# Optimization experiments

Measured on AMD Instinct MI355X. Metric: run time of the kernel, lower is better.

Reference implementation:

```python
import jax, jax.numpy as jnp
import numpy as np

N, E, D, H = 10000, 160000, 128, 4  # nodes, edges, node/edge dim, heads
HC = H * D  # 512, concat output dim of TransformerConv
LN_EPS = 1e-5


def setup_inputs() -> dict:
    key = jax.random.key(0)
    ks = jax.random.split(key, 16)
    s = 1.0 / np.sqrt(D)
    s2 = 1.0 / np.sqrt(HC)
    return {
        "x": jax.random.normal(ks[0], (N, D), jnp.float32),
        "edge_index": jax.random.randint(ks[1], (2, E), 0, N, jnp.int64),
        "edge_attr": jax.random.normal(ks[2], (E, D), jnp.float32),
        "Wq": jax.random.normal(ks[3], (D, HC), jnp.float32) * s,
        "bq": jnp.zeros((HC,), jnp.float32),
        "Wk": jax.random.normal(ks[4], (D, HC), jnp.float32) * s,
        "bk": jnp.zeros((HC,), jnp.float32),
        "Wv": jax.random.normal(ks[5], (D, HC), jnp.float32) * s,
        "bv": jnp.zeros((HC,), jnp.float32),
        "We": jax.random.normal(ks[6], (D, HC), jnp.float32) * s,
        "be": jnp.zeros((HC,), jnp.float32),
        "Wskip": jax.random.normal(ks[7], (D, HC), jnp.float32) * s,
        "bskip": jnp.zeros((HC,), jnp.float32),
        "ln_g": jnp.ones((HC,), jnp.float32),
        "ln_b": jnp.zeros((HC,), jnp.float32),
        "Wlin": jax.random.normal(ks[8], (HC, D), jnp.float32) * s2,
        "blin": jnp.zeros((D,), jnp.float32),
    }


def reference(x, edge_index, edge_attr, Wq, bq, Wk, bk, Wv, bv, We, be,
              Wskip, bskip, ln_g, ln_b, Wlin, blin):
    n = x.shape[0]
    src, dst = edge_index[0], edge_index[1]  # message flows src -> dst
    q = (x @ Wq + bq).reshape(n, H, D)
    k = (x @ Wk + bk).reshape(n, H, D)
    v = (x @ Wv + bv).reshape(n, H, D)
    e = (edge_attr @ We + be).reshape(-1, H, D)  # [E,H,D]

    kj = k[src] + e                                   # [E,H,D]
    alpha = jnp.einsum('ehd,ehd->eh', q[dst], kj) / np.sqrt(D)  # [E,H]
    # per-destination-node, per-head softmax over incoming edges
    amax = jax.ops.segment_max(alpha, dst, num_segments=n)      # [N,H]
    ex = jnp.exp(alpha - amax[dst])
    denom = jax.ops.segment_sum(ex, dst, num_segments=n)        # [N,H]
    attn = ex / denom[dst]                                      # [E,H]

    msg = (v[src] + e) * attn[:, :, None]                       # [E,H,D]
    agg = jax.ops.segment_sum(msg, dst, num_segments=n).reshape(n, HC)
    out = agg + (x @ Wskip + bskip)  # root/skip connection (concat heads)

    # LayerNorm over H*D
    mu = out.mean(-1, keepdims=True)
    var = ((out - mu) ** 2).mean(-1, keepdims=True)
    normed = (out - mu) * jax.lax.rsqrt(var + LN_EPS) * ln_g + ln_b

    lin = normed @ Wlin + blin
    return jax.nn.elu(lin + x)
```

## Files before the change

kernel.cpp:

```cpp
#include <hip/hip_runtime.h>
#include <math.h>


typedef short bf16x8 __attribute__((ext_vector_type(8)));
typedef unsigned short u16x8 __attribute__((ext_vector_type(8)));
typedef float f32x4 __attribute__((ext_vector_type(4)));

#define SCALE 0.08838834764831845f

__device__ inline unsigned short f2bf(float f) {
    union { float f; unsigned u; } v; v.f = f;
    unsigned r = (v.u + 0x7FFFu + ((v.u >> 16) & 1u)) >> 16;
    return (unsigned short)r;
}
__device__ inline float bf2f(unsigned short u) {
    union { unsigned u; float f; } v; v.u = ((unsigned)u) << 16; return v.f;
}

__global__ __launch_bounds__(256) void wqe_k(
    const float* __restrict__ Wq, const float* __restrict__ bq,
    const float* __restrict__ We,
    float* __restrict__ WqeT, float* __restrict__ bqe)
{
    const int b = blockIdx.x;
    if (b < 256) {
        const int gid = b * 256 + threadIdx.x;
        const int m = gid >> 9, hc = gid & 511;
        const int h = hc >> 7, c = hc & 127;
        const float* wq = &Wq[(size_t)m * 512 + h * 128];
        const float* we = &We[(size_t)c * 512 + h * 128];
        float s0 = 0.f, s1 = 0.f;
        #pragma unroll 8
        for (int d = 0; d < 128; d += 2) { s0 += wq[d] * we[d]; s1 += wq[d + 1] * we[d + 1]; }
        WqeT[(size_t)m * 512 + hc] = (s0 + s1) * SCALE;
    } else {
        const int hc = (b - 256) * 256 + threadIdx.x;
        const int h = hc >> 7, c = hc & 127;
        const float* we = &We[(size_t)c * 512 + h * 128];
        const float* bb = &bq[h * 128];
        float s = 0.f;
        #pragma unroll 8
        for (int d = 0; d < 128; ++d) s += bb[d] * we[d];
        bqe[hc] = s * SCALE;
    }
}

__global__ __launch_bounds__(256) void prep_k(
    const float* __restrict__ x,
    const float* __restrict__ Wq, const float* __restrict__ bq,
    const float* __restrict__ Wk, const float* __restrict__ bk,
    const float* __restrict__ Wv, const float* __restrict__ bv,
    const float* __restrict__ Ws, const float* __restrict__ bs,
    const float* __restrict__ WqeT, const float* __restrict__ bqe,
    const float* __restrict__ We, const float* __restrict__ Wlin,
    unsigned short* __restrict__ x_bf, unsigned short* __restrict__ Wfrag,
    unsigned short* __restrict__ Wefrag, unsigned short* __restrict__ Wlfrag,
    float* __restrict__ bcat, int n, int nb1)
{
    const int b = blockIdx.x, t = threadIdx.x;
    if (b < nb1) {
        int i = (b * 256 + t) * 4;
        if (i < n * 128) {
            float4 v = *(const float4*)&x[i];
            unsigned short o[4] = { f2bf(v.x), f2bf(v.y), f2bf(v.z), f2bf(v.w) };
            *(uint2*)&x_bf[i] = *(uint2*)o;
        }
    } else if (b < nb1 + 160) {
        int g = (b - nb1) * 256 + t;
        int lane = g & 63, kt = (g >> 6) & 3, nt = g >> 8;
        int ncol = nt * 16 + (lane & 15);
        int k0 = kt * 32 + ((lane >> 4) << 3);
        const float* W; int c; float sc = 1.f;
        if      (ncol < 512)  { W = Wq;   c = ncol; sc = SCALE; }
        else if (ncol < 1024) { W = Wk;   c = ncol - 512; }
        else if (ncol < 1536) { W = Wv;   c = ncol - 1024; }
        else if (ncol < 2048) { W = Ws;   c = ncol - 1536; }
        else                  { W = WqeT; c = ncol - 2048; }
        unsigned short o[8];
        #pragma unroll
        for (int j = 0; j < 8; ++j) o[j] = f2bf(W[(size_t)(k0 + j) * 512 + c] * sc);
        *(uint4*)&Wfrag[(size_t)g * 8] = *(uint4*)o;
    } else if (b < nb1 + 192) {
        int g = (b - nb1 - 160) * 256 + t;
        int lane = g & 63, kt = (g >> 6) & 3, nt = g >> 8;
        int ncol = nt * 16 + (lane & 15);
        int k0 = kt * 32 + ((lane >> 4) << 3);
        unsigned short o[8];
        #pragma unroll
        for (int j = 0; j < 8; ++j) o[j] = f2bf(We[(size_t)(k0 + j) * 512 + ncol]);
        *(uint4*)&Wefrag[(size_t)g * 8] = *(uint4*)o;
    } else if (b < nb1 + 224) {
        int g = (b - nb1 - 192) * 256 + t;
        int lane = g & 63, kt = (g >> 6) & 15, nt = g >> 10;
        int ncol = nt * 16 + (lane & 15);
        int k0 = kt * 32 + ((lane >> 4) << 3);
        unsigned short o[8];
        #pragma unroll
        for (int j = 0; j < 8; ++j) o[j] = f2bf(Wlin[(size_t)(k0 + j) * 128 + ncol]);
        *(uint4*)&Wlfrag[(size_t)g * 8] = *(uint4*)o;
    } else {
        int c = (b - nb1 - 224) * 256 + t;
        if (c < 2560)
            bcat[c] = (c < 512) ? bq[c] * SCALE : (c < 1024) ? bk[c - 512]
                     : (c < 1536) ? bv[c - 1024] : (c < 2048) ? bs[c - 1536] : bqe[c - 2048];
    }
}

__global__ __launch_bounds__(256) void node_gemm_mfma(
    const unsigned short* __restrict__ x_bf, const unsigned short* __restrict__ Wfrag,
    const float* __restrict__ bcat, float* __restrict__ qs,
    unsigned short* __restrict__ kvq, int n)
{
    const int t = threadIdx.x, lane = t & 63, w = t >> 6;
    const int m0 = blockIdx.x * 64 + (w >> 1) * 32;
    const int n0 = blockIdx.y * 64 + (w & 1) * 32;
    const int lr = lane & 15, lk = (lane >> 4) << 3;
    f32x4 acc[2][2] = {};
    #pragma unroll
    for (int kt = 0; kt < 4; ++kt) {
        bf16x8 a[2], bf[2];
        #pragma unroll
        for (int mi = 0; mi < 2; ++mi) {
            int row = m0 + mi * 16 + lr; row = row < n ? row : n - 1;
            a[mi] = *(const bf16x8*)&x_bf[(size_t)row * 128 + kt * 32 + lk];
        }
        #pragma unroll
        for (int ni = 0; ni < 2; ++ni) {
            int nt = (n0 + ni * 16) >> 4;
            bf[ni] = *(const bf16x8*)&Wfrag[(size_t)((nt * 4 + kt) * 64 + lane) * 8];
        }
        #pragma unroll
        for (int mi = 0; mi < 2; ++mi)
            #pragma unroll
            for (int ni = 0; ni < 2; ++ni)
                acc[mi][ni] = __builtin_amdgcn_mfma_f32_16x16x32_bf16(a[mi], bf[ni], acc[mi][ni], 0, 0, 0);
    }
    #pragma unroll
    for (int mi = 0; mi < 2; ++mi)
        #pragma unroll
        for (int j = 0; j < 4; ++j) {
            int row = m0 + mi * 16 + (lane >> 4) * 4 + j;
            if (row < n) {
                #pragma unroll
                for (int ni = 0; ni < 2; ++ni) {
                    int col = n0 + ni * 16 + lr;
                    float val = acc[mi][ni][j] + bcat[col];
                    if (col < 1536)       kvq[(size_t)row * 2048 + col] = f2bf(val);
                    else if (col < 2048)  qs[(size_t)row * 512 + col - 1536] = val;
                    else                  kvq[(size_t)row * 2048 + col - 512] = f2bf(val);
                }
            }
        }
}

__global__ void deg_count_k(const int* __restrict__ dst, int* __restrict__ deg, int E)
{
    int e = blockIdx.x * 256 + threadIdx.x;
    if (e < E) atomicAdd(&deg[dst[e]], 1);
}

__global__ __launch_bounds__(1024) void scan_k(const int* __restrict__ deg,
                                               int* __restrict__ row_start,
                                               int* __restrict__ cursor, int n)
{
    __shared__ int part[1024];
    const int t = threadIdx.x;
    const int c0 = t * 16;
    int loc[16];
    int s = 0;
    #pragma unroll
    for (int i = 0; i < 16; ++i) {
        int idx = c0 + i;
        int dv = (idx < n) ? deg[idx] : 0;
        loc[i] = s; s += dv;
    }
    part[t] = s;
    __syncthreads();
    int incl = s;
    for (int off = 1; off < 1024; off <<= 1) {
        int other = (t >= off) ? part[t - off] : 0;
        __syncthreads();
        incl += other;
        part[t] = incl;
        __syncthreads();
    }
    const int base = incl - s;
    #pragma unroll
    for (int i = 0; i < 16; ++i) {
        int idx = c0 + i;
        if (idx < n) { row_start[idx] = base + loc[i]; cursor[idx] = base + loc[i]; }
    }
    if (t == 1023) row_start[n] = incl;
}

__global__ void scatter_k(const int* __restrict__ ei, int* __restrict__ cursor,
                          int2* __restrict__ csr, int E)
{
    int e = blockIdx.x * 256 + threadIdx.x;
    if (e < E) {
        int dnode = ei[E + e];
        int p = atomicAdd(&cursor[dnode], 1);
        csr[p] = make_int2(e, ei[e]);
    }
}

__global__ __launch_bounds__(256) void edge_k(
    const unsigned short* __restrict__ kvq, const float* __restrict__ ea,
    const float* __restrict__ be,
    const int* __restrict__ row_start, const int2* __restrict__ csr,
    unsigned short* __restrict__ wsum_bf, unsigned short* __restrict__ vacc_bf, int n)
{
    const int t = threadIdx.x, lane = t & 63, w = t >> 6;
    const int slot = w >> 1, half = w & 1;
    const int node = blockIdx.x * 2 + slot;
    const bool nvalid = node < n;
    const int nodec = nvalid ? node : 0;
    const int g = lane >> 4;
    const int l15 = lane & 15;
    const int sl = l15 * 8;

    __shared__ float lds_m[2][4], lds_den[2][4];
    __shared__ float lds_va[2][4][128], lds_ws[2][4][128];

    int rs = 0, deg = 0;
    if (nvalid) { rs = row_start[node]; deg = row_start[node + 1] - rs; }
    const int dh = (deg + 1) >> 1;
    const int lo = half ? dh : 0;
    const int myc = half ? (deg - dh) : dh;

    float q8[8], qe8[8];
    {
        const u16x8 uq  = *(const u16x8*)&kvq[(size_t)nodec * 2048 + g * 128 + sl];
        const u16x8 uqe = *(const u16x8*)&kvq[(size_t)nodec * 2048 + 1536 + g * 128 + sl];
        #pragma unroll
        for (int i = 0; i < 8; ++i) { q8[i] = bf2f(uq[i]); qe8[i] = bf2f(uqe[i]); }
    }
    float qbe;
    {
        const float* bp = &be[g * 128 + sl];
        float pb = 0.f;
        #pragma unroll
        for (int i = 0; i < 8; ++i) pb += q8[i] * bp[i];
        #pragma unroll
        for (int o = 1; o <= 8; o <<= 1) pb += __shfl_xor(pb, o);
        qbe = pb;
    }

    float m = -3.0e38f, den = 0.f;
    float va[8] = {}, ws[8] = {};

    for (int j0 = 0; j0 < myc; j0 += 64) {
        const int cnt = min(64, myc - j0);
        int2 my = make_int2(0, 0);
        if (lane < cnt) my = csr[rs + lo + j0 + lane];
        for (int jj = 0; jj < cnt; jj += 2) {
            const bool two = (jj + 1 < cnt);
            const int j1 = two ? jj + 1 : jj;
            const int eid0 = __shfl(my.x, jj), src0 = __shfl(my.y, jj);
            const int eid1 = __shfl(my.x, j1), src1 = __shfl(my.y, j1);
            const float* ep0 = &ea[(size_t)eid0 * 128 + sl];
            const float* ep1 = &ea[(size_t)eid1 * 128 + sl];
            float4 eA0 = *(const float4*)ep0, eB0 = *(const float4*)(ep0 + 4);
            float4 eA1 = *(const float4*)ep1, eB1 = *(const float4*)(ep1 + 4);
            const u16x8 k0 = *(const u16x8*)&kvq[(size_t)src0 * 2048 + 512 + g * 128 + sl];
            const u16x8 v0 = *(const u16x8*)&kvq[(size_t)src0 * 2048 + 1024 + g * 128 + sl];
            const u16x8 k1 = *(const u16x8*)&kvq[(size_t)src1 * 2048 + 512 + g * 128 + sl];
            const u16x8 v1 = *(const u16x8*)&kvq[(size_t)src1 * 2048 + 1024 + g * 128 + sl];
            float ef0[8] = {eA0.x, eA0.y, eA0.z, eA0.w, eB0.x, eB0.y, eB0.z, eB0.w};
            float ef1[8] = {eA1.x, eA1.y, eA1.z, eA1.w, eB1.x, eB1.y, eB1.z, eB1.w};
            float p0 = 0.f, p1 = 0.f;
            #pragma unroll
            for (int i = 0; i < 8; ++i) {
                p0 += q8[i] * bf2f(k0[i]) + qe8[i] * ef0[i];
                p1 += q8[i] * bf2f(k1[i]) + qe8[i] * ef1[i];
            }
            #pragma unroll
            for (int o = 1; o <= 8; o <<= 1) {
                p0 += __shfl_xor(p0, o);
                p1 += __shfl_xor(p1, o);
            }
            const float a0 = p0 + qbe;
            const float a1 = two ? (p1 + qbe) : -3.0e38f;
            const float gm = fmaxf(a0, a1);
            if (gm > m + 8.f) {
                const float sc = __expf(m - gm);
                den *= sc;
                #pragma unroll
                for (int i = 0; i < 8; ++i) { va[i] *= sc; ws[i] *= sc; }
                m = gm;
            }
            const float w0 = __expf(a0 - m);
            const float w1 = __expf(a1 - m);
            den += w0 + w1;
            #pragma unroll
            for (int i = 0; i < 8; ++i) {
                va[i] += w0 * bf2f(v0[i]) + w1 * bf2f(v1[i]);
                ws[i] += w0 * ef0[i] + w1 * ef1[i];
            }
        }
    }

    if (half == 1) {
        if (l15 == 0) { lds_m[slot][g] = m; lds_den[slot][g] = den; }
        #pragma unroll
        for (int i = 0; i < 8; ++i) {
            lds_va[slot][g][sl + i] = va[i];
            lds_ws[slot][g][sl + i] = ws[i];
        }
    }
    __syncthreads();
    if (half == 0 && nvalid) {
        const float m1 = lds_m[slot][g], den1 = lds_den[slot][g];
        const float M = fmaxf(m, m1);
        const float s0 = __expf(m - M), s1 = __expf(m1 - M);
        const float dtot = den * s0 + den1 * s1;
        const float rden = (dtot > 0.f) ? 1.f / dtot : 0.f;
        unsigned short vo[8], wo[8];
        #pragma unroll
        for (int i = 0; i < 8; ++i) {
            vo[i] = f2bf((va[i] * s0 + lds_va[slot][g][sl + i] * s1) * rden);
            wo[i] = f2bf((ws[i] * s0 + lds_ws[slot][g][sl + i] * s1) * rden);
        }
        *(uint4*)&vacc_bf[(size_t)node * 512 + g * 128 + sl] = *(uint4*)vo;
        *(uint4*)&wsum_bf[(size_t)node * 512 + g * 128 + sl] = *(uint4*)wo;
    }
}

__global__ __launch_bounds__(256) void tail_k(
    const unsigned short* __restrict__ wsum_bf, const unsigned short* __restrict__ Wefrag,
    const float* __restrict__ be, const unsigned short* __restrict__ vacc_bf,
    const float* __restrict__ qs, const int* __restrict__ row_start,
    const unsigned short* __restrict__ Wlfrag, const float* __restrict__ lng,
    const float* __restrict__ lnb, const float* __restrict__ blin,
    const float* __restrict__ x, float* __restrict__ out, int n)
{
    const int t = threadIdx.x, lane = t & 63, w = t >> 6;
    const int r0 = blockIdx.x * 16;
    const int lr = lane & 15, lk = (lane >> 4) << 3;
    __shared__ unsigned short nlds[16][520];
    __shared__ float red_s[4][16], red_q[4][16], mval[16], rval[16];

    f32x4 acc[8] = {};
    #pragma unroll
    for (int kt = 0; kt < 4; ++kt) {
        int row = r0 + lr; row = row < n ? row : n - 1;
        bf16x8 a = *(const bf16x8*)&wsum_bf[(size_t)row * 512 + w * 128 + kt * 32 + lk];
        #pragma unroll
        for (int ni = 0; ni < 8; ++ni) {
            bf16x8 bfr = *(const bf16x8*)&Wefrag[(size_t)(((w * 8 + ni) * 4 + kt) * 64 + lane) * 8];
            acc[ni] = __builtin_amdgcn_mfma_f32_16x16x32_bf16(a, bfr, acc[ni], 0, 0, 0);
        }
    }
    float g8[8], b8[8];
    #pragma unroll
    for (int ni = 0; ni < 8; ++ni) { int col = w * 128 + ni * 16 + lr; g8[ni] = lng[col]; b8[ni] = lnb[col]; }
    float sum_[4], sq_[4];
    #pragma unroll
    for (int j = 0; j < 4; ++j) {
        int row = r0 + (lane >> 4) * 4 + j;
        int rowc = row < n ? row : n - 1;
        const float hb = (row_start[rowc + 1] > row_start[rowc]) ? 1.f : 0.f;
        float s = 0.f, q = 0.f;
        #pragma unroll
        for (int ni = 0; ni < 8; ++ni) {
            int col = w * 128 + ni * 16 + lr;
            float y = acc[ni][j] + bf2f(vacc_bf[(size_t)rowc * 512 + col]) + hb * be[col]
                    + qs[(size_t)rowc * 512 + col];
            acc[ni][j] = y;
            s += y; q += y * y;
        }
        sum_[j] = s; sq_[j] = q;
    }
    #pragma unroll
    for (int o = 1; o <= 8; o <<= 1) {
        #pragma unroll
        for (int j = 0; j < 4; ++j) { sum_[j] += __shfl_xor(sum_[j], o); sq_[j] += __shfl_xor(sq_[j], o); }
    }
    if (lr == 0) {
        #pragma unroll
        for (int j = 0; j < 4; ++j) {
            red_s[w][(lane >> 4) * 4 + j] = sum_[j];
            red_q[w][(lane >> 4) * 4 + j] = sq_[j];
        }
    }
    __syncthreads();
    if (t < 16) {
        float S = red_s[0][t] + red_s[1][t] + red_s[2][t] + red_s[3][t];
        float Q = red_q[0][t] + red_q[1][t] + red_q[2][t] + red_q[3][t];
        float mu = S * (1.f / 512.f);
        float var = Q * (1.f / 512.f) - mu * mu;
        mval[t] = mu;
        rval[t] = rsqrtf(fmaxf(var, 0.f) + 1e-5f);
    }
    __syncthreads();
    #pragma unroll
    for (int j = 0; j < 4; ++j) {
        int rowl = (lane >> 4) * 4 + j;
        float mu = mval[rowl], rv = rval[rowl];
        #pragma unroll
        for (int ni = 0; ni < 8; ++ni) {
            int col = w * 128 + ni * 16 + lr;
            nlds[rowl][col] = f2bf((acc[ni][j] - mu) * rv * g8[ni] + b8[ni]);
        }
    }
    __syncthreads();
    f32x4 acc2[2] = {};
    #pragma unroll
    for (int kt = 0; kt < 16; ++kt) {
        bf16x8 a2 = *(const bf16x8*)&nlds[lr][kt * 32 + lk];
        #pragma unroll
        for (int ni = 0; ni < 2; ++ni) {
            bf16x8 bfr = *(const bf16x8*)&Wlfrag[(size_t)(((w * 2 + ni) * 16 + kt) * 64 + lane) * 8];
            acc2[ni] = __builtin_amdgcn_mfma_f32_16x16x32_bf16(a2, bfr, acc2[ni], 0, 0, 0);
        }
    }
    #pragma unroll
    for (int j = 0; j < 4; ++j) {
        int row = r0 + (lane >> 4) * 4 + j;
        if (row < n) {
            #pragma unroll
            for (int ni = 0; ni < 2; ++ni) {
                int col = w * 32 + ni * 16 + lr;
                float z = acc2[ni][j] + blin[col] + x[(size_t)row * 128 + col];
                out[(size_t)row * 128 + col] = z > 0.f ? z : expm1f(z);
            }
        }
    }
}

extern "C" void kernel_launch(void* const* d_in, const int* in_sizes, int n_in,
                              void* d_out, int out_size, void* d_ws, size_t ws_size,
                              hipStream_t stream)
{
    const float* x   = (const float*)d_in[0];
    const int*   ei  = (const int*)d_in[1];
    const float* ea  = (const float*)d_in[2];
    const float* Wq  = (const float*)d_in[3];
    const float* bq  = (const float*)d_in[4];
    const float* Wk  = (const float*)d_in[5];
    const float* bk  = (const float*)d_in[6];
    const float* Wv  = (const float*)d_in[7];
    const float* bv  = (const float*)d_in[8];
    const float* We  = (const float*)d_in[9];
    const float* be  = (const float*)d_in[10];
    const float* Wsk = (const float*)d_in[11];
    const float* bsk = (const float*)d_in[12];
    const float* lng = (const float*)d_in[13];
    const float* lnb = (const float*)d_in[14];
    const float* Wl  = (const float*)d_in[15];
    const float* bl  = (const float*)d_in[16];
    float* out = (float*)d_out;

    const int n = in_sizes[0] / 128;
    const int E = in_sizes[1] / 2;

    float* qs    = (float*)d_ws;
    float* WqeT  = qs + (size_t)n * 512;
    float* bqe   = WqeT + 128 * 512;
    float* bcat  = bqe + 512;
    unsigned short* x_bf    = (unsigned short*)(bcat + 2560);
    unsigned short* wsum_bf = x_bf + (size_t)n * 128;
    unsigned short* vacc_bf = wsum_bf + (size_t)n * 512;
    unsigned short* kvq     = vacc_bf + (size_t)n * 512;
    unsigned short* Wfrag   = kvq + (size_t)n * 2048;
    unsigned short* Wefrag  = Wfrag + 128 * 2560;
    unsigned short* Wlfrag  = Wefrag + 128 * 512;
    int2* csr = (int2*)(((uintptr_t)(Wlfrag + 512 * 128) + 7) & ~(uintptr_t)7);
    int* deg       = (int*)(csr + E);
    int* row_start = deg + n;
    int* cursor    = row_start + n + 1;

    hipMemsetAsync(deg, 0, (size_t)n * sizeof(int), stream);

    wqe_k<<<258, 256, 0, stream>>>(Wq, bq, We, WqeT, bqe);
    const int nb1 = (n * 32 + 255) / 256;
    prep_k<<<nb1 + 234, 256, 0, stream>>>(x, Wq, bq, Wk, bk, Wv, bv, Wsk, bsk, WqeT, bqe,
                                          We, Wl, x_bf, Wfrag, Wefrag, Wlfrag, bcat, n, nb1);
    dim3 g1((n + 63) / 64, 40);
    node_gemm_mfma<<<g1, 256, 0, stream>>>(x_bf, Wfrag, bcat, qs, kvq, n);
    deg_count_k<<<(E + 255) / 256, 256, 0, stream>>>(ei + E, deg, E);
    scan_k<<<1, 1024, 0, stream>>>(deg, row_start, cursor, n);
    scatter_k<<<(E + 255) / 256, 256, 0, stream>>>(ei, cursor, csr, E);
    edge_k<<<(n + 1) / 2, 256, 0, stream>>>(kvq, ea, be, row_start, csr,
                                            wsum_bf, vacc_bf, n);
    tail_k<<<(n + 15) / 16, 256, 0, stream>>>(wsum_bf, Wefrag, be, vacc_bf, qs, row_start,
                                              Wlfrag, lng, lnb, bl, x, out, n);
}
```

Measured before the change: 181.2 us.

## Fold CSR build into existing kernels and unroll edge loop by four

```diff
diff --git a/kernel.cpp b/kernel.cpp
--- a/kernel.cpp
+++ b/kernel.cpp
@@ -20,7 +20,8 @@
 __global__ __launch_bounds__(256) void wqe_k(
     const float* __restrict__ Wq, const float* __restrict__ bq,
     const float* __restrict__ We,
-    float* __restrict__ WqeT, float* __restrict__ bqe)
+    float* __restrict__ WqeT, float* __restrict__ bqe,
+    int* __restrict__ deg, int n)
 {
     const int b = blockIdx.x;
     if (b < 256) {
@@ -33,7 +34,7 @@
         #pragma unroll 8
         for (int d = 0; d < 128; d += 2) { s0 += wq[d] * we[d]; s1 += wq[d + 1] * we[d + 1]; }
         WqeT[(size_t)m * 512 + hc] = (s0 + s1) * SCALE;
-    } else {
+    } else if (b < 258) {
         const int hc = (b - 256) * 256 + threadIdx.x;
         const int h = hc >> 7, c = hc & 127;
         const float* we = &We[(size_t)c * 512 + h * 128];
@@ -42,6 +43,9 @@
         #pragma unroll 8
         for (int d = 0; d < 128; ++d) s += bb[d] * we[d];
         bqe[hc] = s * SCALE;
+    } else {
+        int idx = (b - 258) * 256 + threadIdx.x;
+        if (idx < n) deg[idx] = 0;
     }
 }
 
@@ -55,7 +59,8 @@
     const float* __restrict__ We, const float* __restrict__ Wlin,
     unsigned short* __restrict__ x_bf, unsigned short* __restrict__ Wfrag,
     unsigned short* __restrict__ Wefrag, unsigned short* __restrict__ Wlfrag,
-    float* __restrict__ bcat, int n, int nb1)
+    float* __restrict__ bcat,
+    const int* __restrict__ ei, int* __restrict__ deg, int E, int n, int nb1)
 {
     const int b = blockIdx.x, t = threadIdx.x;
     if (b < nb1) {
@@ -98,19 +103,67 @@
         #pragma unroll
         for (int j = 0; j < 8; ++j) o[j] = f2bf(Wlin[(size_t)(k0 + j) * 128 + ncol]);
         *(uint4*)&Wlfrag[(size_t)g * 8] = *(uint4*)o;
-    } else {
+    } else if (b < nb1 + 234) {
         int c = (b - nb1 - 224) * 256 + t;
         if (c < 2560)
             bcat[c] = (c < 512) ? bq[c] * SCALE : (c < 1024) ? bk[c - 512]
                      : (c < 1536) ? bv[c - 1024] : (c < 2048) ? bs[c - 1536] : bqe[c - 2048];
-    }
+    } else {
+        int e = (b - nb1 - 234) * 256 + t;
+        if (e < E) atomicAdd(&deg[ei[E + e]], 1);
+    }
+}
+
+__global__ __launch_bounds__(1024) void scan_k(const int* __restrict__ deg,
+                                               int* __restrict__ row_start,
+                                               int* __restrict__ cursor, int n)
+{
+    __shared__ int part[1024];
+    const int t = threadIdx.x;
+    const int c0 = t * 16;
+    int loc[16];
+    int s = 0;
+    #pragma unroll
+    for (int i = 0; i < 16; ++i) {
+        int idx = c0 + i;
+        int dv = (idx < n) ? deg[idx] : 0;
+        loc[i] = s; s += dv;
+    }
+    part[t] = s;
+    __syncthreads();
+    int incl = s;
+    for (int off = 1; off < 1024; off <<= 1) {
+        int other = (t >= off) ? part[t - off] : 0;
+        __syncthreads();
+        incl += other;
+        part[t] = incl;
+        __syncthreads();
+    }
+    const int base = incl - s;
+    #pragma unroll
+    for (int i = 0; i < 16; ++i) {
+        int idx = c0 + i;
+        if (idx < n) { row_start[idx] = base + loc[i]; cursor[idx] = base + loc[i]; }
+    }
+    if (t == 1023) row_start[n] = incl;
 }
 
 __global__ __launch_bounds__(256) void node_gemm_mfma(
     const unsigned short* __restrict__ x_bf, const unsigned short* __restrict__ Wfrag,
     const float* __restrict__ bcat, float* __restrict__ qs,
-    unsigned short* __restrict__ kvq, int n)
-{
+    unsigned short* __restrict__ kvq,
+    const int* __restrict__ ei, int* __restrict__ cursor, int2* __restrict__ csr,
+    int E, int n)
+{
+    if (blockIdx.y == 40) {
+        const int nth = gridDim.x * 256;
+        for (int e = blockIdx.x * 256 + threadIdx.x; e < E; e += nth) {
+            int dnode = ei[E + e];
+            int p = atomicAdd(&cursor[dnode], 1);
+            csr[p] = make_int2(e, ei[e]);
+        }
+        return;
+    }
     const int t = threadIdx.x, lane = t & 63, w = t >> 6;
     const int m0 = blockIdx.x * 64 + (w >> 1) * 32;
     const int n0 = blockIdx.y * 64 + (w & 1) * 32;
@@ -153,58 +206,7 @@
         }
 }
 
-__global__ void deg_count_k(const int* __restrict__ dst, int* __restrict__ deg, int E)
-{
-    int e = blockIdx.x * 256 + threadIdx.x;
-    if (e < E) atomicAdd(&deg[dst[e]], 1);
-}
-
-__global__ __launch_bounds__(1024) void scan_k(const int* __restrict__ deg,
-                                               int* __restrict__ row_start,
-                                               int* __restrict__ cursor, int n)
-{
-    __shared__ int part[1024];
-    const int t = threadIdx.x;
-    const int c0 = t * 16;
-    int loc[16];
-    int s = 0;
-    #pragma unroll
-    for (int i = 0; i < 16; ++i) {
-        int idx = c0 + i;
-        int dv = (idx < n) ? deg[idx] : 0;
-        loc[i] = s; s += dv;
-    }
-    part[t] = s;
-    __syncthreads();
-    int incl = s;
-    for (int off = 1; off < 1024; off <<= 1) {
-        int other = (t >= off) ? part[t - off] : 0;
-        __syncthreads();
-        incl += other;
-        part[t] = incl;
-        __syncthreads();
-    }
-    const int base = incl - s;
-    #pragma unroll
-    for (int i = 0; i < 16; ++i) {
-        int idx = c0 + i;
-        if (idx < n) { row_start[idx] = base + loc[i]; cursor[idx] = base + loc[i]; }
-    }
-    if (t == 1023) row_start[n] = incl;
-}
-
-__global__ void scatter_k(const int* __restrict__ ei, int* __restrict__ cursor,
-                          int2* __restrict__ csr, int E)
-{
-    int e = blockIdx.x * 256 + threadIdx.x;
-    if (e < E) {
-        int dnode = ei[E + e];
-        int p = atomicAdd(&cursor[dnode], 1);
-        csr[p] = make_int2(e, ei[e]);
-    }
-}
-
-__global__ __launch_bounds__(256) void edge_k(
+__global__ __launch_bounds__(256, 4) void edge_k(
     const unsigned short* __restrict__ kvq, const float* __restrict__ ea,
     const float* __restrict__ be,
     const int* __restrict__ row_start, const int2* __restrict__ csr,
@@ -253,35 +255,51 @@
         const int cnt = min(64, myc - j0);
         int2 my = make_int2(0, 0);
         if (lane < cnt) my = csr[rs + lo + j0 + lane];
-        for (int jj = 0; jj < cnt; jj += 2) {
-            const bool two = (jj + 1 < cnt);
-            const int j1 = two ? jj + 1 : jj;
-            const int eid0 = __shfl(my.x, jj), src0 = __shfl(my.y, jj);
-            const int eid1 = __shfl(my.x, j1), src1 = __shfl(my.y, j1);
-            const float* ep0 = &ea[(size_t)eid0 * 128 + sl];
-            const float* ep1 = &ea[(size_t)eid1 * 128 + sl];
-            float4 eA0 = *(const float4*)ep0, eB0 = *(const float4*)(ep0 + 4);
-            float4 eA1 = *(const float4*)ep1, eB1 = *(const float4*)(ep1 + 4);
-            const u16x8 k0 = *(const u16x8*)&kvq[(size_t)src0 * 2048 + 512 + g * 128 + sl];
-            const u16x8 v0 = *(const u16x8*)&kvq[(size_t)src0 * 2048 + 1024 + g * 128 + sl];
-            const u16x8 k1 = *(const u16x8*)&kvq[(size_t)src1 * 2048 + 512 + g * 128 + sl];
-            const u16x8 v1 = *(const u16x8*)&kvq[(size_t)src1 * 2048 + 1024 + g * 128 + sl];
-            float ef0[8] = {eA0.x, eA0.y, eA0.z, eA0.w, eB0.x, eB0.y, eB0.z, eB0.w};
-            float ef1[8] = {eA1.x, eA1.y, eA1.z, eA1.w, eB1.x, eB1.y, eB1.z, eB1.w};
-            float p0 = 0.f, p1 = 0.f;
+        for (int jj = 0; jj < cnt; jj += 4) {
+            const int i1 = min(jj + 1, cnt - 1), i2 = min(jj + 2, cnt - 1), i3 = min(jj + 3, cnt - 1);
+            const bool b1 = jj + 1 < cnt, b2 = jj + 2 < cnt, b3 = jj + 3 < cnt;
+            const int e0 = __shfl(my.x, jj), s0_ = __shfl(my.y, jj);
+            const int e1 = __shfl(my.x, i1), s1_ = __shfl(my.y, i1);
+            const int e2 = __shfl(my.x, i2), s2_ = __shfl(my.y, i2);
+            const int e3 = __shfl(my.x, i3), s3_ = __shfl(my.y, i3);
+            const float* ep0 = &ea[(size_t)e0 * 128 + sl];
+            const float* ep1 = &ea[(size_t)e1 * 128 + sl];
+            const float* ep2 = &ea[(size_t)e2 * 128 + sl];
+            const float* ep3 = &ea[(size_t)e3 * 128 + sl];
+            float4 A0 = *(const float4*)ep0, B0 = *(const float4*)(ep0 + 4);
+            float4 A1 = *(const float4*)ep1, B1 = *(const float4*)(ep1 + 4);
+            float4 A2 = *(const float4*)ep2, B2 = *(const float4*)(ep2 + 4);
+            float4 A3 = *(const float4*)ep3, B3 = *(const float4*)(ep3 + 4);
+            const u16x8 K0 = *(const u16x8*)&kvq[(size_t)s0_ * 2048 + 512 + g * 128 + sl];
+            const u16x8 V0 = *(const u16x8*)&kvq[(size_t)s0_ * 2048 + 1024 + g * 128 + sl];
+            const u16x8 K1 = *(const u16x8*)&kvq[(size_t)s1_ * 2048 + 512 + g * 128 + sl];
+            const u16x8 V1 = *(const u16x8*)&kvq[(size_t)s1_ * 2048 + 1024 + g * 128 + sl];
+            const u16x8 K2 = *(const u16x8*)&kvq[(size_t)s2_ * 2048 + 512 + g * 128 + sl];
+            const u16x8 V2 = *(const u16x8*)&kvq[(size_t)s2_ * 2048 + 1024 + g * 128 + sl];
+            const u16x8 K3 = *(const u16x8*)&kvq[(size_t)s3_ * 2048 + 512 + g * 128 + sl];
+            const u16x8 V3 = *(const u16x8*)&kvq[(size_t)s3_ * 2048 + 1024 + g * 128 + sl];
+            float ef0[8] = {A0.x, A0.y, A0.z, A0.w, B0.x, B0.y, B0.z, B0.w};
+            float ef1[8] = {A1.x, A1.y, A1.z, A1.w, B1.x, B1.y, B1.z, B1.w};
+            float ef2[8] = {A2.x, A2.y, A2.z, A2.w, B2.x, B2.y, B2.z, B2.w};
+            float ef3[8] = {A3.x, A3.y, A3.z, A3.w, B3.x, B3.y, B3.z, B3.w};
+            float p0 = 0.f, p1 = 0.f, p2 = 0.f, p3 = 0.f;
             #pragma unroll
             for (int i = 0; i < 8; ++i) {
-                p0 += q8[i] * bf2f(k0[i]) + qe8[i] * ef0[i];
-                p1 += q8[i] * bf2f(k1[i]) + qe8[i] * ef1[i];
+                p0 += q8[i] * bf2f(K0[i]) + qe8[i] * ef0[i];
+                p1 += q8[i] * bf2f(K1[i]) + qe8[i] * ef1[i];
+                p2 += q8[i] * bf2f(K2[i]) + qe8[i] * ef2[i];
+                p3 += q8[i] * bf2f(K3[i]) + qe8[i] * ef3[i];
             }
             #pragma unroll
             for (int o = 1; o <= 8; o <<= 1) {
-                p0 += __shfl_xor(p0, o);
-                p1 += __shfl_xor(p1, o);
+                p0 += __shfl_xor(p0, o); p1 += __shfl_xor(p1, o);
+                p2 += __shfl_xor(p2, o); p3 += __shfl_xor(p3, o);
             }
             const float a0 = p0 + qbe;
-            const float a1 = two ? (p1 + qbe) : -3.0e38f;
-            const float gm = fmaxf(a0, a1);
+            const float a1 = b1 ? (p1 + qbe) : -3.0e38f;
+            const float a2 = b2 ? (p2 + qbe) : -3.0e38f;
+            const float a3 = b3 ? (p3 + qbe) : -3.0e38f;
+            const float gm = fmaxf(fmaxf(a0, a1), fmaxf(a2, a3));
             if (gm > m + 8.f) {
                 const float sc = __expf(m - gm);
                 den *= sc;
@@ -291,11 +309,13 @@
             }
             const float w0 = __expf(a0 - m);
             const float w1 = __expf(a1 - m);
-            den += w0 + w1;
+            const float w2 = __expf(a2 - m);
+            const float w3 = __expf(a3 - m);
+            den += (w0 + w1) + (w2 + w3);
             #pragma unroll
             for (int i = 0; i < 8; ++i) {
-                va[i] += w0 * bf2f(v0[i]) + w1 * bf2f(v1[i]);
-                ws[i] += w0 * ef0[i] + w1 * ef1[i];
+                va[i] += (w0 * bf2f(V0[i]) + w1 * bf2f(V1[i])) + (w2 * bf2f(V2[i]) + w3 * bf2f(V3[i]));
+                ws[i] += (w0 * ef0[i] + w1 * ef1[i]) + (w2 * ef2[i] + w3 * ef3[i]);
             }
         }
     }
@@ -470,17 +490,16 @@
     int* row_start = deg + n;
     int* cursor    = row_start + n + 1;
 
-    hipMemsetAsync(deg, 0, (size_t)n * sizeof(int), stream);
-
-    wqe_k<<<258, 256, 0, stream>>>(Wq, bq, We, WqeT, bqe);
+    const int ndegb = (n + 255) / 256;
+    wqe_k<<<258 + ndegb, 256, 0, stream>>>(Wq, bq, We, WqeT, bqe, deg, n);
     const int nb1 = (n * 32 + 255) / 256;
-    prep_k<<<nb1 + 234, 256, 0, stream>>>(x, Wq, bq, Wk, bk, Wv, bv, Wsk, bsk, WqeT, bqe,
-                                          We, Wl, x_bf, Wfrag, Wefrag, Wlfrag, bcat, n, nb1);
-    dim3 g1((n + 63) / 64, 40);
-    node_gemm_mfma<<<g1, 256, 0, stream>>>(x_bf, Wfrag, bcat, qs, kvq, n);
-    deg_count_k<<<(E + 255) / 256, 256, 0, stream>>>(ei + E, deg, E);
+    const int ndc = (E + 255) / 256;
+    prep_k<<<nb1 + 234 + ndc, 256, 0, stream>>>(x, Wq, bq, Wk, bk, Wv, bv, Wsk, bsk, WqeT, bqe,
+                                                We, Wl, x_bf, Wfrag, Wefrag, Wlfrag, bcat,
+                                                ei, deg, E, n, nb1);
     scan_k<<<1, 1024, 0, stream>>>(deg, row_start, cursor, n);
-    scatter_k<<<(E + 255) / 256, 256, 0, stream>>>(ei, cursor, csr, E);
+    dim3 g1((n + 63) / 64, 41);
+    node_gemm_mfma<<<g1, 256, 0, stream>>>(x_bf, Wfrag, bcat, qs, kvq, ei, cursor, csr, E, n);
     edge_k<<<(n + 1) / 2, 256, 0, stream>>>(kvq, ea, be, row_start, csr,
                                             wsum_bf, vacc_bf, n);
     tail_k<<<(n + 15) / 16, 256, 0, stream>>>(wsum_bf, Wefrag, be, vacc_bf, qs, row_start,
```

After: 181.2 us. About the same (-0.0%).
